# Kernel optimization log

Measured on AMD Instinct MI355X. Metric: run time of the kernel, lower is better.

The kernel has to match this reference:

```python
import jax, jax.numpy as jnp
import numpy as np

B, SD, AD, H, QE, NQ = 16384, 512, 64, 1024, 64, 64


def setup_inputs() -> dict:
    key = jax.random.key(0)
    ks = jax.random.split(key, 12)
    s = 0.02
    p = lambda k, shape: (jax.random.normal(k, shape, jnp.float32) * s)
    return {
        "state": jax.random.normal(ks[0], (B, SD), jnp.float32),
        "action": jax.random.normal(ks[1], (B, AD), jnp.float32),
        # twin critics: leading axis 2 stacks q1 / q2 parameters
        "W_e1": p(ks[2], (2, QE, 1)),      "b_e1": p(ks[3], (2, QE)),
        "W_e2": p(ks[4], (2, QE, QE)),     "b_e2": p(ks[5], (2, QE)),
        "W_f1": p(ks[6], (2, H, SD + AD)), "b_f1": p(ks[7], (2, H)),
        "g1": jnp.ones((2, H), jnp.float32),  "beta1": jnp.zeros((2, H), jnp.float32),
        "W_f2": p(ks[8], (2, H, H)),       "b_f2": p(ks[9], (2, H)),
        "g2": jnp.ones((2, H), jnp.float32),  "beta2": jnp.zeros((2, H), jnp.float32),
        "W_h": p(ks[10], (2, 1, H + QE)),  "b_h": p(ks[11], (2, 1)),
    }


def _layernorm(x, g, b, eps=1e-5):
    mu = x.mean(-1, keepdims=True)
    var = ((x - mu) ** 2).mean(-1, keepdims=True)
    return (x - mu) * jax.lax.rsqrt(var + eps) * g + b


def _qnet(state, action, W_e1, b_e1, W_e2, b_e2, W_f1, b_f1, g1, beta1,
          W_f2, b_f2, g2, beta2, W_h, b_h):
    # feature_net (eval mode: dropout is identity)
    x = jnp.concatenate([state, action], axis=-1)            # [B, SD+AD]
    h = jax.nn.relu(_layernorm(x @ W_f1.T + b_f1, g1, beta1))
    feat = jax.nn.relu(_layernorm(h @ W_f2.T + b_f2, g2, beta2))  # [B, H]
    # tau embedding (batch-independent -> compute once per quantile, not per sample)
    tau = (jnp.linspace(0.0, 1.0, NQ + 1)[:-1] + 1.0 / (2 * NQ))[:, None]  # [NQ,1]
    te = jax.nn.relu(tau @ W_e1.T + b_e1) @ W_e2.T + b_e2    # [NQ, QE]
    # head on concat([feat, te]) == linear split (exact same math as the 64-iter loop)
    q_feat = feat @ W_h[0, :H]                               # [B]
    q_tau = te @ W_h[0, H:]                                  # [NQ]
    return q_feat[:, None] + q_tau[None, :] + b_h[0]         # [B, NQ]


def reference(state, action, W_e1, b_e1, W_e2, b_e2, W_f1, b_f1, g1, beta1,
              W_f2, b_f2, g2, beta2, W_h, b_h):
    qnet = lambda *ps: _qnet(state, action, *ps)
    q = jax.vmap(qnet)(W_e1, b_e1, W_e2, b_e2, W_f1, b_f1, g1, beta1,
                       W_f2, b_f2, g2, beta2, W_h, b_h)      # [2, B, NQ]
    return q[0], q[1]
```

## Files before the change

### kernel.cpp

```cpp
#include <hip/hip_runtime.h>
#include <stdint.h>

#define BATCH 16384
#define SDIM 512
#define ADIM 64
#define XDIM 576
#define HDIM 1024
#define NQD 64
#define QED 64

typedef __attribute__((ext_vector_type(8))) short short8;
typedef __attribute__((ext_vector_type(4))) float f32x4;

static __device__ inline unsigned short f2bf(float f) {
  unsigned int u = __float_as_uint(f);
  unsigned int r = (u + 0x7fffu + ((u >> 16) & 1u)) >> 16;
  return (unsigned short)r;
}
static __device__ inline float bf2f(unsigned short u) {
  return __uint_as_float(((unsigned int)u) << 16);
}

static __device__ inline void gload_lds16(const void* g, void* l) {
  __builtin_amdgcn_global_load_lds(
      (const __attribute__((address_space(1))) uint32_t*)g,
      (__attribute__((address_space(3))) uint32_t*)l, 16, 0, 0);
}


__global__ __launch_bounds__(256) void prep_all(const float* __restrict__ st,
                                                const float* __restrict__ ac,
                                                unsigned short* __restrict__ xb,
                                                const float* __restrict__ w1s,
                                                unsigned short* __restrict__ w1d,
                                                const float* __restrict__ w2s,
                                                unsigned short* __restrict__ w2d,
                                                const float* __restrict__ We1,
                                                const float* __restrict__ be1,
                                                const float* __restrict__ We2,
                                                const float* __restrict__ be2,
                                                const float* __restrict__ Wh,
                                                const float* __restrict__ bh,
                                                float* __restrict__ qtau) {
  const int bid = (int)blockIdx.x;
  if (bid >= 2048) {
    const int u = (bid - 2048) * 4 + ((int)threadIdx.x >> 6);
    const int c = u >> 6;
    const int nq = u & 63;
    const int q = (int)threadIdx.x & 63;
    const float tau = (float)nq / 64.0f + 0.0078125f;
    float acc = be2[c * 64 + q];
    for (int e = 0; e < 64; ++e) {
      const float t1 = fmaxf(tau * We1[c * 64 + e] + be1[c * 64 + e], 0.0f);
      acc += t1 * We2[(c * 64 + q) * 64 + e];
    }
    float v = acc * Wh[c * (HDIM + QED) + HDIM + q];
    #pragma unroll
    for (int off = 32; off; off >>= 1) v += __shfl_xor(v, off);
    if (q == 0) qtau[c * 64 + nq] = v + bh[c];
    return;
  }
  const int nx = BATCH * XDIM / 4;
  const int n1 = 2 * HDIM * XDIM / 4;
  const int n2 = 2 * HDIM * HDIM / 4;
  for (int i = bid * 256 + (int)threadIdx.x; i < nx + n1 + n2; i += 2048 * 256) {
    float4 v;
    unsigned short* dst;
    int di;
    if (i < nx) {
      const int e = i * 4;
      const int b = e / XDIM;
      const int j = e - b * XDIM;
      if (j < SDIM) v = *(const float4*)(st + (size_t)b * SDIM + j);
      else          v = *(const float4*)(ac + (size_t)b * ADIM + (j - SDIM));
      dst = xb; di = i;
    } else if (i < nx + n1) {
      di = i - nx; v = ((const float4*)w1s)[di]; dst = w1d;
    } else {
      di = i - nx - n1; v = ((const float4*)w2s)[di]; dst = w2d;
    }
    ushort4 o;
    o.x = f2bf(v.x); o.y = f2bf(v.y); o.z = f2bf(v.z); o.w = f2bf(v.w);
    ((ushort4*)dst)[di] = o;
  }
}


template <int K>
__global__ __launch_bounds__(512, 4) void gemm_bc(const unsigned short* __restrict__ Abase,
                                                  size_t aCritStride,
                                                  const unsigned short* __restrict__ Wbase,
                                                  const float* __restrict__ biasBase,
                                                  unsigned short* __restrict__ Cbase) {
  constexpr int NT = K / 32;
  __shared__ unsigned short As[2][256][32];
  __shared__ unsigned short Bs[2][128][32];

  const int tid  = threadIdx.x;
  const int lane = tid & 63;
  const int wave = tid >> 6;
  const int wm = wave >> 1;
  const int wn = wave & 1;

  const int bid = (int)blockIdx.x;
  const int L = (bid & 7) * 128 + (bid >> 3);
  const int n = L & 7;
  const int cidx = (L >> 3) & 1;
  const int m = L >> 4;
  const int mBase = m * 256;
  const int nBase = n * 128;

  const unsigned short* A = Abase + aCritStride * (size_t)cidx;
  const unsigned short* W = Wbase + (size_t)cidx * HDIM * K;
  const float* bias = biasBase + cidx * HDIM;
  unsigned short* C = Cbase + (size_t)cidx * BATCH * HDIM;

  auto stage = [&](int buf, int kt) {
    #pragma unroll
    for (int i = 0; i < 2; ++i) {
      const int flat = i * 512 + tid;
      const int row  = flat >> 2;
      const int ls   = (flat & 3) ^ ((row >> 1) & 3);
      gload_lds16(A + (size_t)(mBase + row) * K + kt * 32 + ls * 8,
                  &As[buf][0][0] + (size_t)flat * 8);
    }
    {
      const int row = tid >> 2;
      const int ls  = (tid & 3) ^ ((row >> 1) & 3);
      gload_lds16(W + (size_t)(nBase + row) * K + kt * 32 + ls * 8,
                  &Bs[buf][0][0] + (size_t)tid * 8);
    }
  };

  f32x4 acc[4][4];
  #pragma unroll
  for (int fm = 0; fm < 4; ++fm)
    #pragma unroll
    for (int fn = 0; fn < 4; ++fn) {
      f32x4 z = {0.f, 0.f, 0.f, 0.f};
      acc[fm][fn] = z;
    }

  stage(0, 0);
  __syncthreads();

  for (int t = 0; t < NT; ++t) {
    const int buf = t & 1;
    if (t + 1 < NT) stage(buf ^ 1, t + 1);

    short8 af[4], bf[4];
    #pragma unroll
    for (int fm = 0; fm < 4; ++fm) {
      const int r  = wm * 64 + fm * 16 + (lane & 15);
      const int ps = (lane >> 4) ^ ((r >> 1) & 3);
      af[fm] = *(const short8*)&As[buf][r][ps * 8];
    }
    #pragma unroll
    for (int fn = 0; fn < 4; ++fn) {
      const int r  = wn * 64 + fn * 16 + (lane & 15);
      const int ps = (lane >> 4) ^ ((r >> 1) & 3);
      bf[fn] = *(const short8*)&Bs[buf][r][ps * 8];
    }

    __builtin_amdgcn_s_setprio(1);
    #pragma unroll
    for (int fm = 0; fm < 4; ++fm)
      #pragma unroll
      for (int fn = 0; fn < 4; ++fn)
        acc[fm][fn] = __builtin_amdgcn_mfma_f32_16x16x32_bf16(af[fm], bf[fn],
                                                              acc[fm][fn], 0, 0, 0);
    __builtin_amdgcn_s_setprio(0);
    __syncthreads();
  }

  __syncthreads();
  unsigned short* patch = ((unsigned short*)&As[0][0][0]) + wave * 2304;

  float bcol[4];
  #pragma unroll
  for (int fn = 0; fn < 4; ++fn)
    bcol[fn] = bias[nBase + wn * 64 + fn * 16 + (lane & 15)];

  const int cBase = nBase + wn * 64;

  #pragma unroll
  for (int p = 0; p < 2; ++p) {
    #pragma unroll
    for (int f2 = 0; f2 < 2; ++f2) {
      const int fm = p * 2 + f2;
      #pragma unroll
      for (int fn = 0; fn < 4; ++fn) {
        const int rl = f2 * 16 + (lane >> 4) * 4;
        const int cl = fn * 16 + (lane & 15);
        #pragma unroll
        for (int j = 0; j < 4; ++j)
          patch[(rl + j) * 72 + cl] = f2bf(acc[fm][fn][j] + bcol[fn]);
      }
    }
    #pragma unroll
    for (int k = 0; k < 4; ++k) {
      const int rl = k * 8 + (lane >> 3);
      const short8 v = *(const short8*)&patch[rl * 72 + (lane & 7) * 8];
      const int rowg = mBase + wm * 64 + p * 32 + rl;
      *(short8*)(C + (size_t)rowg * HDIM + cBase + (lane & 7) * 8) = v;
    }
  }
}


template <bool HEAD>
__global__ __launch_bounds__(256) void ln_bc(const unsigned short* __restrict__ Xb,
                                             const float* __restrict__ gB,
                                             const float* __restrict__ btB,
                                             unsigned short* __restrict__ Yb,
                                             const float* __restrict__ WhB,
                                             const float* __restrict__ qtB,
                                             float* __restrict__ outB) {
  const int gr = (int)blockIdx.x * 4 + ((int)threadIdx.x >> 6);
  const int c = gr >> 14;
  const int lane = (int)threadIdx.x & 63;

  const unsigned short* X = Xb + (size_t)gr * HDIM + lane * 16;
  const float* g   = gB + c * HDIM + lane * 16;
  const float* bta = btB + c * HDIM + lane * 16;

  const short8 v0 = *(const short8*)(X);
  const short8 v1 = *(const short8*)(X + 8);
  float x[16];
  #pragma unroll
  for (int j = 0; j < 8; ++j) {
    x[j]     = bf2f((unsigned short)v0[j]);
    x[8 + j] = bf2f((unsigned short)v1[j]);
  }
  float s = 0.f, q = 0.f;
  #pragma unroll
  for (int j = 0; j < 16; ++j) { s += x[j]; q += x[j] * x[j]; }
  #pragma unroll
  for (int off = 32; off; off >>= 1) {
    s += __shfl_xor(s, off);
    q += __shfl_xor(q, off);
  }
  const float mu = s * (1.0f / 1024.0f);
  const float var = q * (1.0f / 1024.0f) - mu * mu;
  const float rsig = rsqrtf(var + 1e-5f);

  float y[16];
  #pragma unroll
  for (int j = 0; j < 16; j += 4) {
    const float4 gv = *(const float4*)(g + j);
    const float4 bv = *(const float4*)(bta + j);
    y[j]     = fmaxf((x[j]     - mu) * rsig * gv.x + bv.x, 0.0f);
    y[j + 1] = fmaxf((x[j + 1] - mu) * rsig * gv.y + bv.y, 0.0f);
    y[j + 2] = fmaxf((x[j + 2] - mu) * rsig * gv.z + bv.z, 0.0f);
    y[j + 3] = fmaxf((x[j + 3] - mu) * rsig * gv.w + bv.w, 0.0f);
  }

  if constexpr (!HEAD) {
    short8 o0, o1;
    #pragma unroll
    for (int j = 0; j < 8; ++j) {
      o0[j] = (short)f2bf(y[j]);
      o1[j] = (short)f2bf(y[8 + j]);
    }
    unsigned short* Y = Yb + (size_t)gr * HDIM + lane * 16;
    *(short8*)(Y)     = o0;
    *(short8*)(Y + 8) = o1;
  } else {
    const float* Wh = WhB + c * (HDIM + QED) + lane * 16;
    float p = 0.f;
    #pragma unroll
    for (int j = 0; j < 16; j += 4) {
      const float4 wv = *(const float4*)(Wh + j);
      p += y[j] * wv.x + y[j + 1] * wv.y + y[j + 2] * wv.z + y[j + 3] * wv.w;
    }
    #pragma unroll
    for (int off = 32; off; off >>= 1) p += __shfl_xor(p, off);
    outB[(size_t)gr * NQD + lane] = p + qtB[c * 64 + lane];
  }
}


extern "C" void kernel_launch(void* const* d_in, const int* in_sizes, int n_in,
                              void* d_out, int out_size, void* d_ws, size_t ws_size,
                              hipStream_t stream) {
  (void)in_sizes; (void)n_in; (void)out_size; (void)ws_size;
  const float* state  = (const float*)d_in[0];
  const float* action = (const float*)d_in[1];
  const float* We1 = (const float*)d_in[2];
  const float* be1 = (const float*)d_in[3];
  const float* We2 = (const float*)d_in[4];
  const float* be2 = (const float*)d_in[5];
  const float* Wf1 = (const float*)d_in[6];
  const float* bW1 = (const float*)d_in[7];
  const float* g1  = (const float*)d_in[8];
  const float* bt1 = (const float*)d_in[9];
  const float* Wf2 = (const float*)d_in[10];
  const float* bW2 = (const float*)d_in[11];
  const float* g2  = (const float*)d_in[12];
  const float* bt2 = (const float*)d_in[13];
  const float* Wh  = (const float*)d_in[14];
  const float* bh  = (const float*)d_in[15];
  float* out = (float*)d_out;

  char* ws = (char*)d_ws;
  unsigned short* xb   = (unsigned short*)(ws);
  unsigned short* w1b  = (unsigned short*)(ws + 18874368);
  unsigned short* w2b  = (unsigned short*)(ws + 21233664);
  float*          qtw  = (float*)(ws + 25427968);
  unsigned short* ha   = (unsigned short*)(ws + 25428480);
  unsigned short* hb   = (unsigned short*)(ws + 92537344);

  prep_all<<<2080, 256, 0, stream>>>(state, action, xb, Wf1, w1b, Wf2, w2b,
                                     We1, be1, We2, be2, Wh, bh, qtw);

  gemm_bc<XDIM><<<1024, 512, 0, stream>>>(xb, 0, w1b, bW1, ha);
  ln_bc<false><<<2 * BATCH / 4, 256, 0, stream>>>(ha, g1, bt1, hb, nullptr, nullptr, nullptr);
  gemm_bc<HDIM><<<1024, 512, 0, stream>>>(hb, (size_t)BATCH * HDIM, w2b, bW2, ha);
  ln_bc<true><<<2 * BATCH / 4, 256, 0, stream>>>(ha, g2, bt2, nullptr, Wh, qtw, out);
}
```

Measured before the change: 190.2 us.

## Triple-buffer GEMM LDS staging with prefetch distance two and explicit vmcnt waits

New measurement: 187.3 us. No clear change (-1.5%).

```diff
diff --git a/kernel.cpp b/kernel.cpp
--- a/kernel.cpp
+++ b/kernel.cpp
@@ -26,6 +26,8 @@
       (const __attribute__((address_space(1))) uint32_t*)g,
       (__attribute__((address_space(3))) uint32_t*)l, 16, 0, 0);
 }
+
+#define FENCE() asm volatile("" ::: "memory")
 
 
 __global__ __launch_bounds__(256) void prep_all(const float* __restrict__ st,
@@ -93,8 +95,8 @@
                                                   const float* __restrict__ biasBase,
                                                   unsigned short* __restrict__ Cbase) {
   constexpr int NT = K / 32;
-  __shared__ unsigned short As[2][256][32];
-  __shared__ unsigned short Bs[2][128][32];
+  __shared__ unsigned short As[3][256][32];
+  __shared__ unsigned short Bs[3][128][32];
 
   const int tid  = threadIdx.x;
   const int lane = tid & 63;
@@ -115,20 +117,20 @@
   const float* bias = biasBase + cidx * HDIM;
   unsigned short* C = Cbase + (size_t)cidx * BATCH * HDIM;
 
-  auto stage = [&](int buf, int kt) {
+  auto stage = [&](int ring, int kt) {
     #pragma unroll
     for (int i = 0; i < 2; ++i) {
       const int flat = i * 512 + tid;
       const int row  = flat >> 2;
       const int ls   = (flat & 3) ^ ((row >> 1) & 3);
       gload_lds16(A + (size_t)(mBase + row) * K + kt * 32 + ls * 8,
-                  &As[buf][0][0] + (size_t)flat * 8);
+                  &As[ring][0][0] + (size_t)flat * 8);
     }
     {
       const int row = tid >> 2;
       const int ls  = (tid & 3) ^ ((row >> 1) & 3);
       gload_lds16(W + (size_t)(nBase + row) * K + kt * 32 + ls * 8,
-                  &Bs[buf][0][0] + (size_t)tid * 8);
+                  &Bs[ring][0][0] + (size_t)tid * 8);
     }
   };
 
@@ -142,24 +144,29 @@
     }
 
   stage(0, 0);
-  __syncthreads();
+  if (NT > 1) stage(1, 1);
+  FENCE();
+  if (NT > 1) asm volatile("s_waitcnt vmcnt(3)" ::: "memory");
+  else        asm volatile("s_waitcnt vmcnt(0)" ::: "memory");
+  __builtin_amdgcn_s_barrier();
+  FENCE();
 
   for (int t = 0; t < NT; ++t) {
-    const int buf = t & 1;
-    if (t + 1 < NT) stage(buf ^ 1, t + 1);
+    const int rt = t % 3;
+    if (t + 2 < NT) stage((t + 2) % 3, t + 2);
 
     short8 af[4], bf[4];
     #pragma unroll
     for (int fm = 0; fm < 4; ++fm) {
       const int r  = wm * 64 + fm * 16 + (lane & 15);
       const int ps = (lane >> 4) ^ ((r >> 1) & 3);
-      af[fm] = *(const short8*)&As[buf][r][ps * 8];
+      af[fm] = *(const short8*)&As[rt][r][ps * 8];
     }
     #pragma unroll
     for (int fn = 0; fn < 4; ++fn) {
       const int r  = wn * 64 + fn * 16 + (lane & 15);
       const int ps = (lane >> 4) ^ ((r >> 1) & 3);
-      bf[fn] = *(const short8*)&Bs[buf][r][ps * 8];
+      bf[fn] = *(const short8*)&Bs[rt][r][ps * 8];
     }
 
     __builtin_amdgcn_s_setprio(1);
@@ -170,10 +177,20 @@
         acc[fm][fn] = __builtin_amdgcn_mfma_f32_16x16x32_bf16(af[fm], bf[fn],
                                                               acc[fm][fn], 0, 0, 0);
     __builtin_amdgcn_s_setprio(0);
-    __syncthreads();
-  }
-
-  __syncthreads();
+
+    if (t + 1 < NT) {
+      FENCE();
+      if (t + 2 < NT) asm volatile("s_waitcnt vmcnt(3)" ::: "memory");
+      else            asm volatile("s_waitcnt vmcnt(0)" ::: "memory");
+      __builtin_amdgcn_s_barrier();
+      FENCE();
+    }
+  }
+
+  FENCE();
+  asm volatile("s_waitcnt vmcnt(0)" ::: "memory");
+  __builtin_amdgcn_s_barrier();
+  FENCE();
   unsigned short* patch = ((unsigned short*)&As[0][0][0]) + wave * 2304;
 
   float bcol[4];
```
